# Kernel optimization log

Measured on AMD Instinct MI355X. Metric: run time of the kernel, lower is better.

Reference implementation:

```python
import jax, jax.numpy as jnp
import numpy as np

# TensorProductConvLayer (DiffDock-style): gather -> edge-MLP-weighted fully
# connected tensor product (lmax=1 irreps) -> scatter-mean.
# in/out irreps: ns x0e + nv x1o + nv x1e + ns x0o ; sh irreps: 1x0e + 1x1o
NS, NV = 16, 4
N_NODES, N_EDGES = 8000, 160000
EDGE_FEAT = 3 * NS                      # 48
IRREPS_DIM = 2 * NS + 6 * NV            # 56
# per-path weight block sizes (fully-connected 'uvw' paths, mul2 = 1):
# [A:0e*0e->0e, B:1o*1o->0e, A:0e*1o->1o, B:1o*0e->1o, C:1e*1o->1o,
#  B:1o*1o->1e, C:1e*0e->1e, D:0o*1o->1e, C:1e*1o->0o, D:0o*0e->0o]
PATH_SIZES = [NS*NS, NV*NS, NS*NV, NV*NV, NV*NV, NV*NV, NV*NV, NS*NV, NV*NS, NS*NS]
W_NUMEL = sum(PATH_SIZES)               # 832
# component-normalized CG factors: 1x1->0 uses delta/sqrt(3); 1x1->1 uses eps/sqrt(2)
INV_SQRT3 = float(1.0 / np.sqrt(3.0))
INV_SQRT2 = float(1.0 / np.sqrt(2.0))
# element path normalization: 1/sqrt(total fan-in mul per output irrep)
A_SCAL = float(1.0 / np.sqrt(NS + NV))      # 0e / 0o outputs
A_VEC = float(1.0 / np.sqrt(NS + 2 * NV))   # 1o / 1e outputs


def setup_inputs() -> dict:
    key = jax.random.key(0)
    ks = jax.random.split(key, 6)
    node_attr = jax.random.normal(ks[0], (N_NODES, IRREPS_DIM), jnp.float32)
    edge_index = jax.random.randint(ks[1], (2, N_EDGES), 0, N_NODES)
    edge_attr = jax.random.normal(ks[2], (N_EDGES, EDGE_FEAT), jnp.float32)
    edge_sh = jax.random.normal(ks[3], (N_EDGES, 4), jnp.float32)
    s = float(1.0 / np.sqrt(EDGE_FEAT))
    fc_w1 = jax.random.normal(ks[4], (EDGE_FEAT, EDGE_FEAT), jnp.float32) * s
    fc_b1 = jnp.zeros((EDGE_FEAT,), jnp.float32)
    fc_w2 = jax.random.normal(ks[5], (EDGE_FEAT, W_NUMEL), jnp.float32) * s
    fc_b2 = jnp.zeros((W_NUMEL,), jnp.float32)
    return dict(node_attr=node_attr, edge_attr=edge_attr, edge_sh=edge_sh,
                fc_w1=fc_w1, fc_b1=fc_b1, fc_w2=fc_w2, fc_b2=fc_b2,
                edge_index=edge_index)


def _split_weights(w):
    outs, off = [], 0
    for sz in PATH_SIZES:
        outs.append(w[:, off:off + sz])
        off += sz
    return outs


def _tp_conv(node_attr, edge_attr, edge_sh, fc_w1, fc_b1, fc_w2, fc_b2, src, dst):
    # edge MLP -> per-edge tensor-product weights [E, 832]
    h = jax.nn.relu(edge_attr @ fc_w1 + fc_b1)
    w = h @ fc_w2 + fc_b2
    wA0, wB0, wA1, wB1, wC1, wB1e, wC1e, wD1e, wC0o, wD0o = _split_weights(w)

    x = node_attr[dst]                         # gather [E, 56]
    x0e = x[:, :NS]
    x1o = x[:, NS:NS + 3 * NV].reshape(-1, NV, 3)
    x1e = x[:, NS + 3 * NV:NS + 6 * NV].reshape(-1, NV, 3)
    x0o = x[:, NS + 6 * NV:]
    s0 = edge_sh[:, 0]
    s1 = edge_sh[:, 1:4]

    # ---- 0e output [E, ns]
    o0e = jnp.einsum('eu,euv->ev', x0e, wA0.reshape(-1, NS, NS)) * s0[:, None]
    dot_b = jnp.einsum('eui,ei->eu', x1o, s1) * INV_SQRT3   # 1o x 1o -> 0e
    o0e = (o0e + jnp.einsum('eu,euv->ev', dot_b, wB0.reshape(-1, NV, NS))) * A_SCAL

    # ---- 1o output [E, nv, 3]
    o1o = jnp.einsum('eu,euv->ev', x0e, wA1.reshape(-1, NS, NV))[:, :, None] * s1[:, None, :]
    o1o = o1o + jnp.einsum('eui,euv->evi', x1o, wB1.reshape(-1, NV, NV)) * s0[:, None, None]
    cr_e = jnp.cross(x1e, s1[:, None, :]) * INV_SQRT2       # 1e x 1o -> 1o
    o1o = (o1o + jnp.einsum('eui,euv->evi', cr_e, wC1.reshape(-1, NV, NV))) * A_VEC

    # ---- 1e output [E, nv, 3]
    cr_o = jnp.cross(x1o, s1[:, None, :]) * INV_SQRT2       # 1o x 1o -> 1e
    o1e = jnp.einsum('eui,euv->evi', cr_o, wB1e.reshape(-1, NV, NV))
    o1e = o1e + jnp.einsum('eui,euv->evi', x1e, wC1e.reshape(-1, NV, NV)) * s0[:, None, None]
    o1e = (o1e + jnp.einsum('eu,euv->ev', x0o, wD1e.reshape(-1, NS, NV))[:, :, None] * s1[:, None, :]) * A_VEC

    # ---- 0o output [E, ns]
    dot_c = jnp.einsum('eui,ei->eu', x1e, s1) * INV_SQRT3   # 1e x 1o -> 0o
    o0o = jnp.einsum('eu,euv->ev', dot_c, wC0o.reshape(-1, NV, NS))
    o0o = (o0o + jnp.einsum('eu,euv->ev', x0o, wD0o.reshape(-1, NS, NS)) * s0[:, None]) * A_SCAL

    tp = jnp.concatenate([o0e, o1o.reshape(-1, 3 * NV), o1e.reshape(-1, 3 * NV), o0o], axis=-1)

    # scatter-mean over source nodes
    summed = jax.ops.segment_sum(tp, src, num_segments=N_NODES)
    counts = jax.ops.segment_sum(jnp.ones((tp.shape[0],), tp.dtype), src, num_segments=N_NODES)
    return summed / jnp.maximum(counts, 1.0)[:, None]


def reference(node_attr, edge_attr, edge_sh, fc_w1, fc_b1, fc_w2, fc_b2, edge_index):
    src, dst = edge_index[0], edge_index[1]
    return _tp_conv(node_attr, edge_attr, edge_sh, fc_w1, fc_b1, fc_w2, fc_b2, src, dst)
```

## Files before the change

### kernel.cpp

```cpp
#include <hip/hip_runtime.h>
#include <hip/hip_fp16.h>

#define IRR    56
#define EF     48
#define WN     832
#define NEDGE  160000
#define NNODE  8000
#define NT     256
#define TE2    64
#define NTASK  (NEDGE / TE2)
#define GRID   512

#define INV_SQRT3 0.5773502691896258f
#define INV_SQRT2 0.7071067811865476f
#define A_SCAL    0.22360679774997896f
#define A_VEC     0.20412414523193154f

typedef __bf16 bf16x8 __attribute__((ext_vector_type(8)));
typedef float  f32x4  __attribute__((ext_vector_type(4)));
typedef unsigned short u16x8 __attribute__((ext_vector_type(8)));
typedef unsigned short u16x4 __attribute__((ext_vector_type(4)));

__device__ __forceinline__ unsigned short f2bf(float f) {
    unsigned int u = __builtin_bit_cast(unsigned int, f);
    u += 0x7FFFu + ((u >> 16) & 1u);
    return (unsigned short)(u >> 16);
}
__device__ __forceinline__ unsigned short f2h(float f) {
    __half h = __float2half(f);
    return __builtin_bit_cast(unsigned short, h);
}
__device__ __forceinline__ float h2f(unsigned short u) {
    __half h = __builtin_bit_cast(__half, u);
    return __half2float(h);
}

__global__ void k_setup(const float* __restrict__ w1, const float* __restrict__ b1,
                        const float* __restrict__ w2, const float* __restrict__ b2,
                        unsigned short* __restrict__ W1T, unsigned short* __restrict__ W2L,
                        const int* __restrict__ edge_index, int* __restrict__ hist)
{
    int o = blockIdx.x * 256 + threadIdx.x;
    if (o < 52 * 2 * 64 * 8) {
        int i = o >> 10;
        int rem = o & 1023;
        int f = rem >> 9;
        int rem2 = rem & 511;
        int l = rem2 >> 3, j = rem2 & 7;
        int mm = l & 15, qq = l >> 4;
        int k = f * 32 + qq * 8 + j;
        int n = i * 16 + mm;
        float v = (k < EF) ? w2[k * WN + n] : ((k == EF) ? b2[n] : 0.f);
        W2L[o] = f2bf(v);
    }
    if (o < EF * EF) { int k = o / EF, n = o - k * EF; W1T[n * 64 + k] = f2bf(w1[o]); }
    if (o < EF * 16) { int n = o >> 4, kk = EF + (o & 15); W1T[n * 64 + kk] = (kk == EF) ? f2bf(b1[n]) : (unsigned short)0; }
    if (o < NEDGE) atomicAdd(&hist[edge_index[o]], 1);
}

__global__ __launch_bounds__(NT, 2) void tp_fused(
    const float* __restrict__ node_attr,
    const float* __restrict__ edge_attr,
    const float* __restrict__ edge_sh,
    const int*   __restrict__ edge_index,
    const int*   __restrict__ hist,
    const unsigned short* __restrict__ W1T,
    const unsigned short* __restrict__ W2L,
    float* __restrict__ out)
{
    __shared__ __align__(16) unsigned short sW2[26 * 1024];
    __shared__ __align__(16) unsigned char  UGH[TE2 * 56 * 4];
    __shared__ __align__(16) unsigned char  UFO[TE2 * 60 * 2];
    __shared__ float sS1[TE2][4];
    __shared__ int   sSrc[TE2], sDst[TE2];
    __shared__ float sInv[TE2];

    float*          sG   = (float*)UGH;
    unsigned short* sH   = (unsigned short*)UGH;
    unsigned short* sF16 = (unsigned short*)UFO;
    float*          sO   = (float*)UFO;

    const int tid    = threadIdx.x;
    const int lane   = tid & 63;
    const int wv     = tid >> 6;
    const int m      = lane & 15;
    const int quad   = lane >> 4;
    const int em     = wv * 16 + m;
    const int flavor = blockIdx.x & 1;
    const int bid2   = blockIdx.x >> 1;

    {
        const uint4* src = (const uint4*)(W2L + (size_t)flavor * 26 * 1024);
        uint4* dst = (uint4*)sW2;
        #pragma unroll
        for (int it = 0; it < 13; it++) dst[it * NT + tid] = src[it * NT + tid];
    }

    for (int task = bid2; task < NTASK; task += 256) {
        const int e0 = task * TE2;
        __syncthreads();
        if (tid < TE2)            sSrc[tid]       = edge_index[e0 + tid];
        else if (tid < 2 * TE2)   sDst[tid - TE2] = edge_index[NEDGE + e0 + tid - TE2];
        __syncthreads();

        {
            const float* nrow = node_attr + (size_t)sDst[em] * IRR;
            float* g = sG + em * 56;
            #pragma unroll
            for (int t = 0; t < 3; t++) {
                int c = quad + t * 4;
                *(float4*)(g + c * 4) = *(const float4*)(nrow + c * 4);
            }
            if (quad < 2) { int c = 12 + quad; *(float4*)(g + c * 4) = *(const float4*)(nrow + c * 4); }
        }
        if (tid >= 128 && tid < 128 + TE2) {
            int e = tid - 128;
            sInv[e] = 1.0f / fmaxf((float)hist[sSrc[e]], 1.0f);
        }
        __syncthreads();

        if (quad == 0) {
            const float* x = sG + em * 56;
            float4 sh4 = *(const float4*)&edge_sh[(size_t)(e0 + em) * 4];
            const float s0 = sh4.x, sx = sh4.y, sy = sh4.z, sz = sh4.w;
            unsigned short* F = sF16 + em * 60;
            const float c0S = s0 * A_SCAL;
            const float c0V = s0 * A_VEC;
            const float cD3 = INV_SQRT3 * A_SCAL;
            const float cC2 = INV_SQRT2 * A_VEC;
            if (flavor == 0) {
                #pragma unroll
                for (int u = 0; u < 16; u++) {
                    float x0e = x[u];
                    F[u]      = f2h(x0e * c0S);
                    F[20 + u] = f2h(x0e * A_VEC);
                }
                #pragma unroll
                for (int u = 0; u < 4; u++) {
                    float a0 = x[16 + u*3], a1 = x[16 + u*3 + 1], a2 = x[16 + u*3 + 2];
                    float b0 = x[28 + u*3], b1 = x[28 + u*3 + 1], b2 = x[28 + u*3 + 2];
                    F[16 + u] = f2h((a0*sx + a1*sy + a2*sz) * cD3);
                    F[36 + u*3 + 0] = f2h(a0 * c0V);
                    F[36 + u*3 + 1] = f2h(a1 * c0V);
                    F[36 + u*3 + 2] = f2h(a2 * c0V);
                    F[48 + u*3 + 0] = f2h((b1*sz - b2*sy) * cC2);
                    F[48 + u*3 + 1] = f2h((b2*sx - b0*sz) * cC2);
                    F[48 + u*3 + 2] = f2h((b0*sy - b1*sx) * cC2);
                }
            } else {
                #pragma unroll
                for (int u = 0; u < 4; u++) {
                    float a0 = x[16 + u*3], a1 = x[16 + u*3 + 1], a2 = x[16 + u*3 + 2];
                    float b0 = x[28 + u*3], b1 = x[28 + u*3 + 1], b2 = x[28 + u*3 + 2];
                    F[u*3 + 0]      = f2h((a1*sz - a2*sy) * cC2);
                    F[u*3 + 1]      = f2h((a2*sx - a0*sz) * cC2);
                    F[u*3 + 2]      = f2h((a0*sy - a1*sx) * cC2);
                    F[12 + u*3 + 0] = f2h(b0 * c0V);
                    F[12 + u*3 + 1] = f2h(b1 * c0V);
                    F[12 + u*3 + 2] = f2h(b2 * c0V);
                    F[40 + u]       = f2h((b0*sx + b1*sy + b2*sz) * cD3);
                }
                #pragma unroll
                for (int u = 0; u < 16; u++) {
                    float x0o = x[40 + u];
                    F[24 + u] = f2h(x0o * A_VEC);
                    F[44 + u] = f2h(x0o * c0S);
                }
            }
            sS1[em][0] = sx; sS1[em][1] = sy; sS1[em][2] = sz;
        }
        __syncthreads();

        {
            const float* arow = edge_attr + (size_t)(e0 + em) * EF;
            float av0[8], av1[8];
            {
                float4 p0 = *(const float4*)(arow + quad * 8);
                float4 p1 = *(const float4*)(arow + quad * 8 + 4);
                av0[0]=p0.x; av0[1]=p0.y; av0[2]=p0.z; av0[3]=p0.w;
                av0[4]=p1.x; av0[5]=p1.y; av0[6]=p1.z; av0[7]=p1.w;
            }
            if (quad < 2) {
                float4 p0 = *(const float4*)(arow + 32 + quad * 8);
                float4 p1 = *(const float4*)(arow + 32 + quad * 8 + 4);
                av1[0]=p0.x; av1[1]=p0.y; av1[2]=p0.z; av1[3]=p0.w;
                av1[4]=p1.x; av1[5]=p1.y; av1[6]=p1.z; av1[7]=p1.w;
            } else {
                #pragma unroll
                for (int j = 0; j < 8; j++) av1[j] = 0.f;
                if (quad == 2) av1[0] = 1.f;
            }
            u16x8 ub0, ub1;
            #pragma unroll
            for (int j = 0; j < 8; j++) { ub0[j] = f2bf(av0[j]); ub1[j] = f2bf(av1[j]); }
            bf16x8 hb0 = __builtin_bit_cast(bf16x8, ub0);
            bf16x8 hb1 = __builtin_bit_cast(bf16x8, ub1);

            #pragma unroll
            for (int nth = 0; nth < 3; nth++) {
                bf16x8 a0 = __builtin_bit_cast(bf16x8, *(const u16x8*)&W1T[(nth*16 + m)*64 + quad*8]);
                bf16x8 a1 = __builtin_bit_cast(bf16x8, *(const u16x8*)&W1T[(nth*16 + m)*64 + 32 + quad*8]);
                f32x4 c = {0.f, 0.f, 0.f, 0.f};
                c = __builtin_amdgcn_mfma_f32_16x16x32_bf16(a0, hb0, c, 0, 0, 0);
                c = __builtin_amdgcn_mfma_f32_16x16x32_bf16(a1, hb1, c, 0, 0, 0);
                u16x4 hp;
                #pragma unroll
                for (int r = 0; r < 4; r++) hp[r] = f2bf(fmaxf(c[r], 0.f));
                *(u16x4*)&sH[em * 72 + nth*16 + quad*4] = hp;
            }
            if (quad == 3) {
                u16x4 b = {0x3F80, 0, 0, 0}, z = {0, 0, 0, 0};
                *(u16x4*)&sH[em * 72 + 48] = b;
                *(u16x4*)&sH[em * 72 + 52] = z;
                *(u16x4*)&sH[em * 72 + 56] = z;
                *(u16x4*)&sH[em * 72 + 60] = z;
            }
        }
        __syncthreads();

        bf16x8 HB0 = __builtin_bit_cast(bf16x8, *(const u16x8*)&sH[em * 72 + quad*8]);
        bf16x8 HB1 = __builtin_bit_cast(bf16x8, *(const u16x8*)&sH[em * 72 + 32 + quad*8]);

        const unsigned short* Fp = sF16 + em * 60;
        const float s1x = sS1[em][0], s1y = sS1[em][1], s1z = sS1[em][2];

        if (flavor == 0) {
            float oe[4] = {0.f,0.f,0.f,0.f};
            float sA[4] = {0.f,0.f,0.f,0.f};
            float t1[12] = {0.f,0.f,0.f,0.f,0.f,0.f,0.f,0.f,0.f,0.f,0.f,0.f};
            #pragma unroll
            for (int i = 0; i < 26; i++) {
                u16x8 Af = *(const u16x8*)&sW2[i * 1024 + lane * 8];
                u16x8 Bf = *(const u16x8*)&sW2[i * 1024 + 512 + lane * 8];
                f32x4 c = {0.f,0.f,0.f,0.f};
                c = __builtin_amdgcn_mfma_f32_16x16x32_bf16(__builtin_bit_cast(bf16x8, Af), HB0, c, 0, 0, 0);
                c = __builtin_amdgcn_mfma_f32_16x16x32_bf16(__builtin_bit_cast(bf16x8, Bf), HB1, c, 0, 0, 0);
                if (i < 20) {
                    float f = h2f(Fp[i]);
                    #pragma unroll
                    for (int r = 0; r < 4; r++) oe[r] += f * c[r];
                } else if (i < 24) {
                    float f = h2f(Fp[20 + (i - 20)*4 + quad]);
                    #pragma unroll
                    for (int r = 0; r < 4; r++) sA[r] += f * c[r];
                } else {
                    int u = (i - 24)*4 + quad;
                    #pragma unroll
                    for (int i3 = 0; i3 < 3; i3++) {
                        float f = h2f(Fp[36 + u*3 + i3]);
                        #pragma unroll
                        for (int r = 0; r < 4; r++) t1[i3*4 + r] += f * c[r];
                    }
                }
            }
            #pragma unroll
            for (int r = 0; r < 4; r++) {
                sA[r] += __shfl_xor(sA[r], 16, 64);  sA[r] += __shfl_xor(sA[r], 32, 64);
            }
            #pragma unroll
            for (int i = 0; i < 12; i++) {
                t1[i] += __shfl_xor(t1[i], 16, 64);  t1[i] += __shfl_xor(t1[i], 32, 64);
            }
            __syncthreads();
            float4 v0; v0.x = oe[0]; v0.y = oe[1]; v0.z = oe[2]; v0.w = oe[3];
            *(float4*)&sO[em * 28 + quad*4] = v0;
            if (quad == 0) {
                #pragma unroll
                for (int r = 0; r < 4; r++) {
                    sO[em * 28 + 16 + r*3 + 0] = sA[r] * s1x + t1[0*4 + r];
                    sO[em * 28 + 16 + r*3 + 1] = sA[r] * s1y + t1[1*4 + r];
                    sO[em * 28 + 16 + r*3 + 2] = sA[r] * s1z + t1[2*4 + r];
                }
            }
        } else {
            float sD[4] = {0.f,0.f,0.f,0.f};
            float t1[12] = {0.f,0.f,0.f,0.f,0.f,0.f,0.f,0.f,0.f,0.f,0.f,0.f};
            float oo[4] = {0.f,0.f,0.f,0.f};
            #pragma unroll
            for (int i = 0; i < 26; i++) {
                u16x8 Af = *(const u16x8*)&sW2[i * 1024 + lane * 8];
                u16x8 Bf = *(const u16x8*)&sW2[i * 1024 + 512 + lane * 8];
                f32x4 c = {0.f,0.f,0.f,0.f};
                c = __builtin_amdgcn_mfma_f32_16x16x32_bf16(__builtin_bit_cast(bf16x8, Af), HB0, c, 0, 0, 0);
                c = __builtin_amdgcn_mfma_f32_16x16x32_bf16(__builtin_bit_cast(bf16x8, Bf), HB1, c, 0, 0, 0);
                if (i < 2) {
                    int j = i*4 + quad;
                    #pragma unroll
                    for (int i3 = 0; i3 < 3; i3++) {
                        float f = h2f(Fp[j*3 + i3]);
                        #pragma unroll
                        for (int r = 0; r < 4; r++) t1[i3*4 + r] += f * c[r];
                    }
                } else if (i < 6) {
                    float f = h2f(Fp[24 + (i - 2)*4 + quad]);
                    #pragma unroll
                    for (int r = 0; r < 4; r++) sD[r] += f * c[r];
                } else {
                    float f = h2f(Fp[40 + (i - 6)]);
                    #pragma unroll
                    for (int r = 0; r < 4; r++) oo[r] += f * c[r];
                }
            }
            #pragma unroll
            for (int r = 0; r < 4; r++) {
                sD[r] += __shfl_xor(sD[r], 16, 64);  sD[r] += __shfl_xor(sD[r], 32, 64);
            }
            #pragma unroll
            for (int i = 0; i < 12; i++) {
                t1[i] += __shfl_xor(t1[i], 16, 64);  t1[i] += __shfl_xor(t1[i], 32, 64);
            }
            __syncthreads();
            float4 v1; v1.x = oo[0]; v1.y = oo[1]; v1.z = oo[2]; v1.w = oo[3];
            *(float4*)&sO[em * 28 + 12 + quad*4] = v1;
            if (quad == 0) {
                #pragma unroll
                for (int r = 0; r < 4; r++) {
                    sO[em * 28 + r*3 + 0] = sD[r] * s1x + t1[0*4 + r];
                    sO[em * 28 + r*3 + 1] = sD[r] * s1y + t1[1*4 + r];
                    sO[em * 28 + r*3 + 2] = sD[r] * s1z + t1[2*4 + r];
                }
            }
        }
        __syncthreads();

        #pragma unroll
        for (int it = 0; it < 7; it++) {
            int idx = it * NT + tid;
            int e = idx / 28, ch = idx - e * 28;
            unsafeAtomicAdd(&out[(size_t)sSrc[e] * IRR + flavor * 28 + ch],
                            sO[e * 28 + ch] * sInv[e]);
        }
    }
}

extern "C" void kernel_launch(void* const* d_in, const int* in_sizes, int n_in,
                              void* d_out, int out_size, void* d_ws, size_t ws_size,
                              hipStream_t stream) {
    const float* node_attr  = (const float*)d_in[0];
    const float* edge_attr  = (const float*)d_in[1];
    const float* edge_sh    = (const float*)d_in[2];
    const float* fc_w1      = (const float*)d_in[3];
    const float* fc_b1      = (const float*)d_in[4];
    const float* fc_w2      = (const float*)d_in[5];
    const float* fc_b2      = (const float*)d_in[6];
    const int*   edge_index = (const int*)d_in[7];

    int* hist = (int*)d_ws;
    unsigned short* W1T = (unsigned short*)(hist + NNODE);
    unsigned short* W2L = W1T + EF * 64;

    hipMemsetAsync(hist, 0, NNODE * sizeof(int), stream);
    hipMemsetAsync(d_out, 0, (size_t)out_size * sizeof(float), stream);

    k_setup<<<(NEDGE + 255) / 256, 256, 0, stream>>>(
        fc_w1, fc_b1, fc_w2, fc_b2, W1T, W2L, edge_index, hist);

    tp_fused<<<GRID, NT, 0, stream>>>(node_attr, edge_attr, edge_sh, edge_index,
                                      hist, W1T, W2L, (float*)d_out);
}
```

Measured before the change: 176.2 us.

## Split edge work into four flavors per block and pre-convert edge_attr to bf16

The persistent two-flavor loop over edge tasks becomes a non-persistent grid with four blocks per 64-edge tile. Each block handles a quarter of the 832 per-edge weights, so the shared W2 slice halves, only the needed node_attr columns are gathered, and the occupancy hint rises from 2 to 3 blocks. Edge attributes are converted to bf16 once in the setup kernel, which now runs 160000*48 threads. The trade-off is that the gather, the first MLP layer and the edge-index loads are repeated four times per tile instead of twice, and the setup kernel writes an extra bf16 copy of edge_attr.

```diff
diff --git a/kernel.cpp b/kernel.cpp
--- a/kernel.cpp
+++ b/kernel.cpp
@@ -7,9 +7,8 @@
 #define NEDGE  160000
 #define NNODE  8000
 #define NT     256
-#define TE2    64
-#define NTASK  (NEDGE / TE2)
-#define GRID   512
+#define EBK    64
+#define GRID   ((NEDGE / EBK) * 4)
 
 #define INV_SQRT3 0.5773502691896258f
 #define INV_SQRT2 0.7071067811865476f
@@ -37,13 +36,15 @@
 
 __global__ void k_setup(const float* __restrict__ w1, const float* __restrict__ b1,
                         const float* __restrict__ w2, const float* __restrict__ b2,
+                        const float* __restrict__ edge_attr, const int* __restrict__ edge_index,
                         unsigned short* __restrict__ W1T, unsigned short* __restrict__ W2L,
-                        const int* __restrict__ edge_index, int* __restrict__ hist)
+                        unsigned short* __restrict__ EAB, int* __restrict__ hist)
 {
-    int o = blockIdx.x * 256 + threadIdx.x;
+    size_t o = (size_t)blockIdx.x * 256 + threadIdx.x;
+    if (o < (size_t)NEDGE * EF) EAB[o] = f2bf(edge_attr[o]);
     if (o < 52 * 2 * 64 * 8) {
-        int i = o >> 10;
-        int rem = o & 1023;
+        int i = (int)(o >> 10);
+        int rem = (int)(o & 1023);
         int f = rem >> 9;
         int rem2 = rem & 511;
         int l = rem2 >> 3, j = rem2 & 7;
@@ -53,282 +54,311 @@
         float v = (k < EF) ? w2[k * WN + n] : ((k == EF) ? b2[n] : 0.f);
         W2L[o] = f2bf(v);
     }
-    if (o < EF * EF) { int k = o / EF, n = o - k * EF; W1T[n * 64 + k] = f2bf(w1[o]); }
-    if (o < EF * 16) { int n = o >> 4, kk = EF + (o & 15); W1T[n * 64 + kk] = (kk == EF) ? f2bf(b1[n]) : (unsigned short)0; }
+    if (o < EF * EF) { int k = (int)o / EF, n = (int)o - k * EF; W1T[n * 64 + k] = f2bf(w1[o]); }
+    if (o < EF * 16) { int n = (int)o >> 4, kk = EF + ((int)o & 15); W1T[n * 64 + kk] = (kk == EF) ? f2bf(b1[n]) : (unsigned short)0; }
     if (o < NEDGE) atomicAdd(&hist[edge_index[o]], 1);
 }
 
-__global__ __launch_bounds__(NT, 2) void tp_fused(
+__global__ __launch_bounds__(NT, 3) void tp_fused(
     const float* __restrict__ node_attr,
-    const float* __restrict__ edge_attr,
     const float* __restrict__ edge_sh,
     const int*   __restrict__ edge_index,
     const int*   __restrict__ hist,
     const unsigned short* __restrict__ W1T,
     const unsigned short* __restrict__ W2L,
+    const unsigned short* __restrict__ EAB,
     float* __restrict__ out)
 {
-    __shared__ __align__(16) unsigned short sW2[26 * 1024];
-    __shared__ __align__(16) unsigned char  UGH[TE2 * 56 * 4];
-    __shared__ __align__(16) unsigned char  UFO[TE2 * 60 * 2];
-    __shared__ float sS1[TE2][4];
-    __shared__ int   sSrc[TE2], sDst[TE2];
-    __shared__ float sInv[TE2];
-
-    float*          sG   = (float*)UGH;
-    unsigned short* sH   = (unsigned short*)UGH;
-    unsigned short* sF16 = (unsigned short*)UFO;
-    float*          sO   = (float*)UFO;
+    __shared__ __align__(16) unsigned short sW2[13 * 1024];
+    __shared__ __align__(16) unsigned char  UGH[EBK * 56 * 4];
+    __shared__ __align__(16) unsigned short sF[EBK * 64];
+    __shared__ float sS1[EBK][4];
+    __shared__ int   sSrc[EBK], sDst[EBK];
+    __shared__ float sInv[EBK];
+
+    float*          sG = (float*)UGH;
+    unsigned short* sH = (unsigned short*)UGH;
+    float*          sO = (float*)sF;
 
     const int tid    = threadIdx.x;
     const int lane   = tid & 63;
     const int wv     = tid >> 6;
     const int m      = lane & 15;
     const int quad   = lane >> 4;
+    const int flavor = blockIdx.x & 3;
+    const int e0     = (blockIdx.x >> 2) * EBK;
     const int em     = wv * 16 + m;
-    const int flavor = blockIdx.x & 1;
-    const int bid2   = blockIdx.x >> 1;
+
+    if (tid < EBK)           sSrc[tid]       = edge_index[e0 + tid];
+    else if (tid < 2 * EBK)  sDst[tid - EBK] = edge_index[NEDGE + e0 + tid - EBK];
+    __syncthreads();
 
     {
-        const uint4* src = (const uint4*)(W2L + (size_t)flavor * 26 * 1024);
+        const uint4* src = (const uint4*)(W2L + (size_t)flavor * 13 * 1024);
         uint4* dst = (uint4*)sW2;
         #pragma unroll
-        for (int it = 0; it < 13; it++) dst[it * NT + tid] = src[it * NT + tid];
-    }
-
-    for (int task = bid2; task < NTASK; task += 256) {
-        const int e0 = task * TE2;
-        __syncthreads();
-        if (tid < TE2)            sSrc[tid]       = edge_index[e0 + tid];
-        else if (tid < 2 * TE2)   sDst[tid - TE2] = edge_index[NEDGE + e0 + tid - TE2];
-        __syncthreads();
-
-        {
-            const float* nrow = node_attr + (size_t)sDst[em] * IRR;
-            float* g = sG + em * 56;
-            #pragma unroll
-            for (int t = 0; t < 3; t++) {
-                int c = quad + t * 4;
-                *(float4*)(g + c * 4) = *(const float4*)(nrow + c * 4);
-            }
-            if (quad < 2) { int c = 12 + quad; *(float4*)(g + c * 4) = *(const float4*)(nrow + c * 4); }
-        }
-        if (tid >= 128 && tid < 128 + TE2) {
-            int e = tid - 128;
-            sInv[e] = 1.0f / fmaxf((float)hist[sSrc[e]], 1.0f);
-        }
-        __syncthreads();
-
+        for (int it = 0; it < 7; it++) {
+            int idx = it * NT + tid;
+            if (idx < 1664) dst[idx] = src[idx];
+        }
+    }
+    if (flavor == 0 || flavor == 3) {
+        int e = tid >> 2, c = tid & 3;
+        int off = (flavor == 0) ? 0 : 40;
+        *(float4*)&sG[e * 56 + off + c * 4] =
+            *(const float4*)&node_attr[(size_t)sDst[e] * IRR + off + c * 4];
+    } else {
+        int off = (flavor == 1) ? 0 : 16;
+        #pragma unroll
+        for (int it = 0; it < 3; it++) {
+            int idx = it * NT + tid;
+            if (idx < 640) {
+                int e = idx / 10, c = idx - e * 10;
+                *(float4*)&sG[e * 56 + off + c * 4] =
+                    *(const float4*)&node_attr[(size_t)sDst[e] * IRR + off + c * 4];
+            }
+        }
+    }
+    if (tid >= 192) {
+        int e = tid - 192;
+        sInv[e] = 1.0f / fmaxf((float)hist[sSrc[e]], 1.0f);
+    }
+    __syncthreads();
+
+    if (quad == 0) {
+        const float* x = sG + em * 56;
+        float4 sh4 = *(const float4*)&edge_sh[(size_t)(e0 + em) * 4];
+        const float s0 = sh4.x, sx = sh4.y, sy = sh4.z, sz = sh4.w;
+        unsigned short* F = sF + em * 64;
+        const float c0S = s0 * A_SCAL;
+        const float c0V = s0 * A_VEC;
+        const float cD3 = INV_SQRT3 * A_SCAL;
+        const float cC2 = INV_SQRT2 * A_VEC;
+        if (flavor == 0) {
+            #pragma unroll
+            for (int u = 0; u < 13; u++) F[u] = f2h(x[u] * c0S);
+        } else if (flavor == 1) {
+            #pragma unroll
+            for (int u = 13; u < 16; u++) F[u] = f2h(x[u] * c0S);
+            #pragma unroll
+            for (int u = 0; u < 16; u++) F[20 + u] = f2h(x[u] * A_VEC);
+            #pragma unroll
+            for (int u = 0; u < 4; u++) {
+                float a0 = x[16+u*3], a1 = x[17+u*3], a2 = x[18+u*3];
+                float b0 = x[28+u*3], b1 = x[29+u*3], b2 = x[30+u*3];
+                F[16 + u] = f2h((a0*sx + a1*sy + a2*sz) * cD3);
+                F[36+u*3+0] = f2h(a0 * c0V);
+                F[36+u*3+1] = f2h(a1 * c0V);
+                F[36+u*3+2] = f2h(a2 * c0V);
+                F[48+u*3+0] = f2h((b1*sz - b2*sy) * cC2);
+                F[48+u*3+1] = f2h((b2*sx - b0*sz) * cC2);
+                F[48+u*3+2] = f2h((b0*sy - b1*sx) * cC2);
+            }
+            sS1[em][0] = sx; sS1[em][1] = sy; sS1[em][2] = sz;
+        } else if (flavor == 2) {
+            #pragma unroll
+            for (int u = 0; u < 4; u++) {
+                float a0 = x[16+u*3], a1 = x[17+u*3], a2 = x[18+u*3];
+                float b0 = x[28+u*3], b1 = x[29+u*3], b2 = x[30+u*3];
+                F[u*3+0] = f2h((a1*sz - a2*sy) * cC2);
+                F[u*3+1] = f2h((a2*sx - a0*sz) * cC2);
+                F[u*3+2] = f2h((a0*sy - a1*sx) * cC2);
+                F[12+u*3+0] = f2h(b0 * c0V);
+                F[12+u*3+1] = f2h(b1 * c0V);
+                F[12+u*3+2] = f2h(b2 * c0V);
+                F[40 + u] = f2h((b0*sx + b1*sy + b2*sz) * cD3);
+            }
+            #pragma unroll
+            for (int u = 0; u < 16; u++) F[24 + u] = f2h(x[40+u] * A_VEC);
+            #pragma unroll
+            for (int u = 0; u < 3; u++)  F[44 + u] = f2h(x[40+u] * c0S);
+            sS1[em][0] = sx; sS1[em][1] = sy; sS1[em][2] = sz;
+        } else {
+            #pragma unroll
+            for (int u = 3; u < 16; u++) F[44 + u] = f2h(x[40+u] * c0S);
+        }
+    }
+    __syncthreads();
+
+    {
+        const unsigned short* ea = EAB + (size_t)(e0 + em) * EF;
+        u16x8 ub0 = *(const u16x8*)(ea + quad * 8);
+        u16x8 ub1 = {0,0,0,0,0,0,0,0};
+        if (quad < 2)       ub1 = *(const u16x8*)(ea + 32 + quad * 8);
+        else if (quad == 2) ub1[0] = 0x3F80;
+        bf16x8 hb0 = __builtin_bit_cast(bf16x8, ub0);
+        bf16x8 hb1 = __builtin_bit_cast(bf16x8, ub1);
+
+        #pragma unroll
+        for (int nth = 0; nth < 3; nth++) {
+            bf16x8 a0 = __builtin_bit_cast(bf16x8, *(const u16x8*)&W1T[(nth*16 + m)*64 + quad*8]);
+            bf16x8 a1 = __builtin_bit_cast(bf16x8, *(const u16x8*)&W1T[(nth*16 + m)*64 + 32 + quad*8]);
+            f32x4 c = {0.f, 0.f, 0.f, 0.f};
+            c = __builtin_amdgcn_mfma_f32_16x16x32_bf16(a0, hb0, c, 0, 0, 0);
+            c = __builtin_amdgcn_mfma_f32_16x16x32_bf16(a1, hb1, c, 0, 0, 0);
+            u16x4 hp;
+            #pragma unroll
+            for (int r = 0; r < 4; r++) hp[r] = f2bf(fmaxf(c[r], 0.f));
+            *(u16x4*)&sH[em * 72 + nth*16 + quad*4] = hp;
+        }
+        if (quad == 3) {
+            u16x4 b = {0x3F80, 0, 0, 0}, z = {0, 0, 0, 0};
+            *(u16x4*)&sH[em * 72 + 48] = b;
+            *(u16x4*)&sH[em * 72 + 52] = z;
+            *(u16x4*)&sH[em * 72 + 56] = z;
+            *(u16x4*)&sH[em * 72 + 60] = z;
+        }
+    }
+    __syncthreads();
+
+    bf16x8 HB0 = __builtin_bit_cast(bf16x8, *(const u16x8*)&sH[em * 72 + quad*8]);
+    bf16x8 HB1 = __builtin_bit_cast(bf16x8, *(const u16x8*)&sH[em * 72 + 32 + quad*8]);
+    const unsigned short* Fp = sF + em * 64;
+
+    if (flavor == 0) {
+        float oe[4] = {0.f,0.f,0.f,0.f};
+        #pragma unroll
+        for (int i = 0; i < 13; i++) {
+            u16x8 Af = *(const u16x8*)&sW2[i * 1024 + lane * 8];
+            u16x8 Bf = *(const u16x8*)&sW2[i * 1024 + 512 + lane * 8];
+            f32x4 c = {0.f,0.f,0.f,0.f};
+            c = __builtin_amdgcn_mfma_f32_16x16x32_bf16(__builtin_bit_cast(bf16x8, Af), HB0, c, 0, 0, 0);
+            c = __builtin_amdgcn_mfma_f32_16x16x32_bf16(__builtin_bit_cast(bf16x8, Bf), HB1, c, 0, 0, 0);
+            float f = h2f(Fp[i]);
+            #pragma unroll
+            for (int r = 0; r < 4; r++) oe[r] += f * c[r];
+        }
+        float4 v; v.x = oe[0]; v.y = oe[1]; v.z = oe[2]; v.w = oe[3];
+        *(float4*)&sO[em * 32 + quad*4] = v;
+    } else if (flavor == 1) {
+        float oe[4] = {0.f,0.f,0.f,0.f};
+        float sA[4] = {0.f,0.f,0.f,0.f};
+        float t1[12] = {0.f,0.f,0.f,0.f,0.f,0.f,0.f,0.f,0.f,0.f,0.f,0.f};
+        #pragma unroll
+        for (int i = 0; i < 13; i++) {
+            u16x8 Af = *(const u16x8*)&sW2[i * 1024 + lane * 8];
+            u16x8 Bf = *(const u16x8*)&sW2[i * 1024 + 512 + lane * 8];
+            f32x4 c = {0.f,0.f,0.f,0.f};
+            c = __builtin_amdgcn_mfma_f32_16x16x32_bf16(__builtin_bit_cast(bf16x8, Af), HB0, c, 0, 0, 0);
+            c = __builtin_amdgcn_mfma_f32_16x16x32_bf16(__builtin_bit_cast(bf16x8, Bf), HB1, c, 0, 0, 0);
+            if (i < 7) {
+                float f = h2f(Fp[13 + i]);
+                #pragma unroll
+                for (int r = 0; r < 4; r++) oe[r] += f * c[r];
+            } else if (i < 11) {
+                float f = h2f(Fp[20 + (i - 7)*4 + quad]);
+                #pragma unroll
+                for (int r = 0; r < 4; r++) sA[r] += f * c[r];
+            } else {
+                int u = (i - 11)*4 + quad;
+                #pragma unroll
+                for (int i3 = 0; i3 < 3; i3++) {
+                    float f = h2f(Fp[36 + u*3 + i3]);
+                    #pragma unroll
+                    for (int r = 0; r < 4; r++) t1[i3*4 + r] += f * c[r];
+                }
+            }
+        }
+        #pragma unroll
+        for (int r = 0; r < 4; r++) {
+            sA[r] += __shfl_xor(sA[r], 16, 64);  sA[r] += __shfl_xor(sA[r], 32, 64);
+        }
+        #pragma unroll
+        for (int i = 0; i < 12; i++) {
+            t1[i] += __shfl_xor(t1[i], 16, 64);  t1[i] += __shfl_xor(t1[i], 32, 64);
+        }
+        float4 v; v.x = oe[0]; v.y = oe[1]; v.z = oe[2]; v.w = oe[3];
+        *(float4*)&sO[em * 32 + quad*4] = v;
         if (quad == 0) {
-            const float* x = sG + em * 56;
-            float4 sh4 = *(const float4*)&edge_sh[(size_t)(e0 + em) * 4];
-            const float s0 = sh4.x, sx = sh4.y, sy = sh4.z, sz = sh4.w;
-            unsigned short* F = sF16 + em * 60;
-            const float c0S = s0 * A_SCAL;
-            const float c0V = s0 * A_VEC;
-            const float cD3 = INV_SQRT3 * A_SCAL;
-            const float cC2 = INV_SQRT2 * A_VEC;
-            if (flavor == 0) {
-                #pragma unroll
-                for (int u = 0; u < 16; u++) {
-                    float x0e = x[u];
-                    F[u]      = f2h(x0e * c0S);
-                    F[20 + u] = f2h(x0e * A_VEC);
+            float s1x = sS1[em][0], s1y = sS1[em][1], s1z = sS1[em][2];
+            #pragma unroll
+            for (int r = 0; r < 4; r++) {
+                sO[em * 32 + 16 + r*3 + 0] = sA[r] * s1x + t1[0*4 + r];
+                sO[em * 32 + 16 + r*3 + 1] = sA[r] * s1y + t1[1*4 + r];
+                sO[em * 32 + 16 + r*3 + 2] = sA[r] * s1z + t1[2*4 + r];
+            }
+        }
+    } else if (flavor == 2) {
+        float sD[4] = {0.f,0.f,0.f,0.f};
+        float t1[12] = {0.f,0.f,0.f,0.f,0.f,0.f,0.f,0.f,0.f,0.f,0.f,0.f};
+        float oo[4] = {0.f,0.f,0.f,0.f};
+        #pragma unroll
+        for (int i = 0; i < 13; i++) {
+            u16x8 Af = *(const u16x8*)&sW2[i * 1024 + lane * 8];
+            u16x8 Bf = *(const u16x8*)&sW2[i * 1024 + 512 + lane * 8];
+            f32x4 c = {0.f,0.f,0.f,0.f};
+            c = __builtin_amdgcn_mfma_f32_16x16x32_bf16(__builtin_bit_cast(bf16x8, Af), HB0, c, 0, 0, 0);
+            c = __builtin_amdgcn_mfma_f32_16x16x32_bf16(__builtin_bit_cast(bf16x8, Bf), HB1, c, 0, 0, 0);
+            if (i < 2) {
+                int j = i*4 + quad;
+                #pragma unroll
+                for (int i3 = 0; i3 < 3; i3++) {
+                    float f = h2f(Fp[j*3 + i3]);
+                    #pragma unroll
+                    for (int r = 0; r < 4; r++) t1[i3*4 + r] += f * c[r];
                 }
-                #pragma unroll
-                for (int u = 0; u < 4; u++) {
-                    float a0 = x[16 + u*3], a1 = x[16 + u*3 + 1], a2 = x[16 + u*3 + 2];
-                    float b0 = x[28 + u*3], b1 = x[28 + u*3 + 1], b2 = x[28 + u*3 + 2];
-                    F[16 + u] = f2h((a0*sx + a1*sy + a2*sz) * cD3);
-                    F[36 + u*3 + 0] = f2h(a0 * c0V);
-                    F[36 + u*3 + 1] = f2h(a1 * c0V);
-                    F[36 + u*3 + 2] = f2h(a2 * c0V);
-                    F[48 + u*3 + 0] = f2h((b1*sz - b2*sy) * cC2);
-                    F[48 + u*3 + 1] = f2h((b2*sx - b0*sz) * cC2);
-                    F[48 + u*3 + 2] = f2h((b0*sy - b1*sx) * cC2);
-                }
+            } else if (i < 6) {
+                float f = h2f(Fp[24 + (i - 2)*4 + quad]);
+                #pragma unroll
+                for (int r = 0; r < 4; r++) sD[r] += f * c[r];
             } else {
-                #pragma unroll
-                for (int u = 0; u < 4; u++) {
-                    float a0 = x[16 + u*3], a1 = x[16 + u*3 + 1], a2 = x[16 + u*3 + 2];
-                    float b0 = x[28 + u*3], b1 = x[28 + u*3 + 1], b2 = x[28 + u*3 + 2];
-                    F[u*3 + 0]      = f2h((a1*sz - a2*sy) * cC2);
-                    F[u*3 + 1]      = f2h((a2*sx - a0*sz) * cC2);
-                    F[u*3 + 2]      = f2h((a0*sy - a1*sx) * cC2);
-                    F[12 + u*3 + 0] = f2h(b0 * c0V);
-                    F[12 + u*3 + 1] = f2h(b1 * c0V);
-                    F[12 + u*3 + 2] = f2h(b2 * c0V);
-                    F[40 + u]       = f2h((b0*sx + b1*sy + b2*sz) * cD3);
-                }
-                #pragma unroll
-                for (int u = 0; u < 16; u++) {
-                    float x0o = x[40 + u];
-                    F[24 + u] = f2h(x0o * A_VEC);
-                    F[44 + u] = f2h(x0o * c0S);
-                }
-            }
-            sS1[em][0] = sx; sS1[em][1] = sy; sS1[em][2] = sz;
-        }
-        __syncthreads();
-
-        {
-            const float* arow = edge_attr + (size_t)(e0 + em) * EF;
-            float av0[8], av1[8];
-            {
-                float4 p0 = *(const float4*)(arow + quad * 8);
-                float4 p1 = *(const float4*)(arow + quad * 8 + 4);
-                av0[0]=p0.x; av0[1]=p0.y; av0[2]=p0.z; av0[3]=p0.w;
-                av0[4]=p1.x; av0[5]=p1.y; av0[6]=p1.z; av0[7]=p1.w;
-            }
-            if (quad < 2) {
-                float4 p0 = *(const float4*)(arow + 32 + quad * 8);
-                float4 p1 = *(const float4*)(arow + 32 + quad * 8 + 4);
-                av1[0]=p0.x; av1[1]=p0.y; av1[2]=p0.z; av1[3]=p0.w;
-                av1[4]=p1.x; av1[5]=p1.y; av1[6]=p1.z; av1[7]=p1.w;
-            } else {
-                #pragma unroll
-                for (int j = 0; j < 8; j++) av1[j] = 0.f;
-                if (quad == 2) av1[0] = 1.f;
-            }
-            u16x8 ub0, ub1;
-            #pragma unroll
-            for (int j = 0; j < 8; j++) { ub0[j] = f2bf(av0[j]); ub1[j] = f2bf(av1[j]); }
-            bf16x8 hb0 = __builtin_bit_cast(bf16x8, ub0);
-            bf16x8 hb1 = __builtin_bit_cast(bf16x8, ub1);
-
-            #pragma unroll
-            for (int nth = 0; nth < 3; nth++) {
-                bf16x8 a0 = __builtin_bit_cast(bf16x8, *(const u16x8*)&W1T[(nth*16 + m)*64 + quad*8]);
-                bf16x8 a1 = __builtin_bit_cast(bf16x8, *(const u16x8*)&W1T[(nth*16 + m)*64 + 32 + quad*8]);
-                f32x4 c = {0.f, 0.f, 0.f, 0.f};
-                c = __builtin_amdgcn_mfma_f32_16x16x32_bf16(a0, hb0, c, 0, 0, 0);
-                c = __builtin_amdgcn_mfma_f32_16x16x32_bf16(a1, hb1, c, 0, 0, 0);
-                u16x4 hp;
-                #pragma unroll
-                for (int r = 0; r < 4; r++) hp[r] = f2bf(fmaxf(c[r], 0.f));
-                *(u16x4*)&sH[em * 72 + nth*16 + quad*4] = hp;
-            }
-            if (quad == 3) {
-                u16x4 b = {0x3F80, 0, 0, 0}, z = {0, 0, 0, 0};
-                *(u16x4*)&sH[em * 72 + 48] = b;
-                *(u16x4*)&sH[em * 72 + 52] = z;
-                *(u16x4*)&sH[em * 72 + 56] = z;
-                *(u16x4*)&sH[em * 72 + 60] = z;
-            }
-        }
-        __syncthreads();
-
-        bf16x8 HB0 = __builtin_bit_cast(bf16x8, *(const u16x8*)&sH[em * 72 + quad*8]);
-        bf16x8 HB1 = __builtin_bit_cast(bf16x8, *(const u16x8*)&sH[em * 72 + 32 + quad*8]);
-
-        const unsigned short* Fp = sF16 + em * 60;
-        const float s1x = sS1[em][0], s1y = sS1[em][1], s1z = sS1[em][2];
-
-        if (flavor == 0) {
-            float oe[4] = {0.f,0.f,0.f,0.f};
-            float sA[4] = {0.f,0.f,0.f,0.f};
-            float t1[12] = {0.f,0.f,0.f,0.f,0.f,0.f,0.f,0.f,0.f,0.f,0.f,0.f};
-            #pragma unroll
-            for (int i = 0; i < 26; i++) {
-                u16x8 Af = *(const u16x8*)&sW2[i * 1024 + lane * 8];
-                u16x8 Bf = *(const u16x8*)&sW2[i * 1024 + 512 + lane * 8];
-                f32x4 c = {0.f,0.f,0.f,0.f};
-                c = __builtin_amdgcn_mfma_f32_16x16x32_bf16(__builtin_bit_cast(bf16x8, Af), HB0, c, 0, 0, 0);
-                c = __builtin_amdgcn_mfma_f32_16x16x32_bf16(__builtin_bit_cast(bf16x8, Bf), HB1, c, 0, 0, 0);
-                if (i < 20) {
-                    float f = h2f(Fp[i]);
-                    #pragma unroll
-                    for (int r = 0; r < 4; r++) oe[r] += f * c[r];
-                } else if (i < 24) {
-                    float f = h2f(Fp[20 + (i - 20)*4 + quad]);
-                    #pragma unroll
-                    for (int r = 0; r < 4; r++) sA[r] += f * c[r];
-                } else {
-                    int u = (i - 24)*4 + quad;
-                    #pragma unroll
-                    for (int i3 = 0; i3 < 3; i3++) {
-                        float f = h2f(Fp[36 + u*3 + i3]);
-                        #pragma unroll
-                        for (int r = 0; r < 4; r++) t1[i3*4 + r] += f * c[r];
-                    }
-                }
-            }
+                float f = h2f(Fp[40 + (i - 6)]);
+                #pragma unroll
+                for (int r = 0; r < 4; r++) oo[r] += f * c[r];
+            }
+        }
+        #pragma unroll
+        for (int r = 0; r < 4; r++) {
+            sD[r] += __shfl_xor(sD[r], 16, 64);  sD[r] += __shfl_xor(sD[r], 32, 64);
+        }
+        #pragma unroll
+        for (int i = 0; i < 12; i++) {
+            t1[i] += __shfl_xor(t1[i], 16, 64);  t1[i] += __shfl_xor(t1[i], 32, 64);
+        }
+        float4 v; v.x = oo[0]; v.y = oo[1]; v.z = oo[2]; v.w = oo[3];
+        *(float4*)&sO[em * 32 + 12 + quad*4] = v;
+        if (quad == 0) {
+            float s1x = sS1[em][0], s1y = sS1[em][1], s1z = sS1[em][2];
             #pragma unroll
             for (int r = 0; r < 4; r++) {
-                sA[r] += __shfl_xor(sA[r], 16, 64);  sA[r] += __shfl_xor(sA[r], 32, 64);
-            }
-            #pragma unroll
-            for (int i = 0; i < 12; i++) {
-                t1[i] += __shfl_xor(t1[i], 16, 64);  t1[i] += __shfl_xor(t1[i], 32, 64);
-            }
-            __syncthreads();
-            float4 v0; v0.x = oe[0]; v0.y = oe[1]; v0.z = oe[2]; v0.w = oe[3];
-            *(float4*)&sO[em * 28 + quad*4] = v0;
-            if (quad == 0) {
-                #pragma unroll
-                for (int r = 0; r < 4; r++) {
-                    sO[em * 28 + 16 + r*3 + 0] = sA[r] * s1x + t1[0*4 + r];
-                    sO[em * 28 + 16 + r*3 + 1] = sA[r] * s1y + t1[1*4 + r];
-                    sO[em * 28 + 16 + r*3 + 2] = sA[r] * s1z + t1[2*4 + r];
-                }
-            }
-        } else {
-            float sD[4] = {0.f,0.f,0.f,0.f};
-            float t1[12] = {0.f,0.f,0.f,0.f,0.f,0.f,0.f,0.f,0.f,0.f,0.f,0.f};
-            float oo[4] = {0.f,0.f,0.f,0.f};
-            #pragma unroll
-            for (int i = 0; i < 26; i++) {
-                u16x8 Af = *(const u16x8*)&sW2[i * 1024 + lane * 8];
-                u16x8 Bf = *(const u16x8*)&sW2[i * 1024 + 512 + lane * 8];
-                f32x4 c = {0.f,0.f,0.f,0.f};
-                c = __builtin_amdgcn_mfma_f32_16x16x32_bf16(__builtin_bit_cast(bf16x8, Af), HB0, c, 0, 0, 0);
-                c = __builtin_amdgcn_mfma_f32_16x16x32_bf16(__builtin_bit_cast(bf16x8, Bf), HB1, c, 0, 0, 0);
-                if (i < 2) {
-                    int j = i*4 + quad;
-                    #pragma unroll
-                    for (int i3 = 0; i3 < 3; i3++) {
-                        float f = h2f(Fp[j*3 + i3]);
-                        #pragma unroll
-                        for (int r = 0; r < 4; r++) t1[i3*4 + r] += f * c[r];
-                    }
-                } else if (i < 6) {
-                    float f = h2f(Fp[24 + (i - 2)*4 + quad]);
-                    #pragma unroll
-                    for (int r = 0; r < 4; r++) sD[r] += f * c[r];
-                } else {
-                    float f = h2f(Fp[40 + (i - 6)]);
-                    #pragma unroll
-                    for (int r = 0; r < 4; r++) oo[r] += f * c[r];
-                }
-            }
-            #pragma unroll
-            for (int r = 0; r < 4; r++) {
-                sD[r] += __shfl_xor(sD[r], 16, 64);  sD[r] += __shfl_xor(sD[r], 32, 64);
-            }
-            #pragma unroll
-            for (int i = 0; i < 12; i++) {
-                t1[i] += __shfl_xor(t1[i], 16, 64);  t1[i] += __shfl_xor(t1[i], 32, 64);
-            }
-            __syncthreads();
-            float4 v1; v1.x = oo[0]; v1.y = oo[1]; v1.z = oo[2]; v1.w = oo[3];
-            *(float4*)&sO[em * 28 + 12 + quad*4] = v1;
-            if (quad == 0) {
-                #pragma unroll
-                for (int r = 0; r < 4; r++) {
-                    sO[em * 28 + r*3 + 0] = sD[r] * s1x + t1[0*4 + r];
-                    sO[em * 28 + r*3 + 1] = sD[r] * s1y + t1[1*4 + r];
-                    sO[em * 28 + r*3 + 2] = sD[r] * s1z + t1[2*4 + r];
-                }
-            }
-        }
-        __syncthreads();
-
+                sO[em * 32 + r*3 + 0] = sD[r] * s1x + t1[0*4 + r];
+                sO[em * 32 + r*3 + 1] = sD[r] * s1y + t1[1*4 + r];
+                sO[em * 32 + r*3 + 2] = sD[r] * s1z + t1[2*4 + r];
+            }
+        }
+    } else {
+        float oo[4] = {0.f,0.f,0.f,0.f};
+        #pragma unroll
+        for (int i = 0; i < 13; i++) {
+            u16x8 Af = *(const u16x8*)&sW2[i * 1024 + lane * 8];
+            u16x8 Bf = *(const u16x8*)&sW2[i * 1024 + 512 + lane * 8];
+            f32x4 c = {0.f,0.f,0.f,0.f};
+            c = __builtin_amdgcn_mfma_f32_16x16x32_bf16(__builtin_bit_cast(bf16x8, Af), HB0, c, 0, 0, 0);
+            c = __builtin_amdgcn_mfma_f32_16x16x32_bf16(__builtin_bit_cast(bf16x8, Bf), HB1, c, 0, 0, 0);
+            float f = h2f(Fp[47 + i]);
+            #pragma unroll
+            for (int r = 0; r < 4; r++) oo[r] += f * c[r];
+        }
+        float4 v; v.x = oo[0]; v.y = oo[1]; v.z = oo[2]; v.w = oo[3];
+        *(float4*)&sO[em * 32 + quad*4] = v;
+    }
+    __syncthreads();
+
+    if (flavor == 1 || flavor == 2) {
+        const int chBase = (flavor == 1) ? 0 : 28;
         #pragma unroll
         for (int it = 0; it < 7; it++) {
             int idx = it * NT + tid;
             int e = idx / 28, ch = idx - e * 28;
-            unsafeAtomicAdd(&out[(size_t)sSrc[e] * IRR + flavor * 28 + ch],
-                            sO[e * 28 + ch] * sInv[e]);
+            unsafeAtomicAdd(&out[(size_t)sSrc[e] * IRR + chBase + ch], sO[e * 32 + ch] * sInv[e]);
+        }
+    } else {
+        const int chBase = (flavor == 0) ? 0 : 40;
+        #pragma unroll
+        for (int it = 0; it < 4; it++) {
+            int idx = it * NT + tid;
+            int e = idx >> 4, ch = idx & 15;
+            unsafeAtomicAdd(&out[(size_t)sSrc[e] * IRR + chBase + ch], sO[e * 32 + ch] * sInv[e]);
         }
     }
 }
@@ -348,13 +378,14 @@
     int* hist = (int*)d_ws;
     unsigned short* W1T = (unsigned short*)(hist + NNODE);
     unsigned short* W2L = W1T + EF * 64;
+    unsigned short* EAB = W2L + 52 * 2 * 64 * 8;
 
     hipMemsetAsync(hist, 0, NNODE * sizeof(int), stream);
     hipMemsetAsync(d_out, 0, (size_t)out_size * sizeof(float), stream);
 
-    k_setup<<<(NEDGE + 255) / 256, 256, 0, stream>>>(
-        fc_w1, fc_b1, fc_w2, fc_b2, W1T, W2L, edge_index, hist);
-
-    tp_fused<<<GRID, NT, 0, stream>>>(node_attr, edge_attr, edge_sh, edge_index,
-                                      hist, W1T, W2L, (float*)d_out);
-}
+    k_setup<<<(NEDGE * EF + 255) / 256, 256, 0, stream>>>(
+        fc_w1, fc_b1, fc_w2, fc_b2, edge_attr, edge_index, W1T, W2L, EAB, hist);
+
+    tp_fused<<<GRID, NT, 0, stream>>>(node_attr, edge_sh, edge_index, hist,
+                                      W1T, W2L, EAB, (float*)d_out);
+}
```

Result: slower. 257.5 us (+46.2%).
